# Kernel optimization log

Measured on AMD Instinct MI355X. Metric: run time of the kernel, lower is better.

Reference implementation:

```python
import jax, jax.numpy as jnp
import numpy as np

T, IN, M, C, OUT = 8192, 1024, 64, 16, 1024  # time, input, trace, context, output


def _ln(x, eps=1e-5):
    mu = jnp.mean(x, axis=-1, keepdims=True)
    var = jnp.var(x, axis=-1, keepdims=True)
    return (x - mu) * jax.lax.rsqrt(var + eps)


def _mish(x):
    return x * jnp.tanh(jax.nn.softplus(x))


def setup_inputs() -> dict:
    key = jax.random.key(0)
    ks = jax.random.split(key, 8)

    def w(k, o, i):
        return (jax.random.normal(k, (o, i), jnp.float32) / np.sqrt(i).astype(np.float32))

    return {
        "x": jax.random.normal(ks[0], (T, IN), jnp.float32),
        "state0": jnp.zeros((1, M, C), jnp.float32),  # real part of complex zero init
        "start": jax.random.uniform(ks[1], (T,)) < 0.002,  # sparse episode resets
        "next_done": jnp.zeros((T,), bool),  # unused by the sequential-equivalent math
        "a": jnp.linspace(1e-6, 0.5, M, dtype=jnp.float32),  # ffa.init decay
        "bf": (2.0 * jnp.pi / jnp.linspace(1.0, 1024.0, C)).astype(jnp.float32),  # ffa.init freqs
        "pre_w": w(ks[2], M, IN), "pre_b": jnp.zeros((M,), jnp.float32),
        "skip_w": w(ks[3], OUT, IN), "skip_b": jnp.zeros((OUT,), jnp.float32),
        "mix_w1": w(ks[4], M * C, 2 * M * C), "mix_b1": jnp.zeros((M * C,), jnp.float32),
        "mix_w2": w(ks[5], M * C, M * C), "mix_b2": jnp.zeros((M * C,), jnp.float32),
        "mix_w3": w(ks[6], OUT, M * C), "mix_b3": jnp.zeros((OUT,), jnp.float32),
    }


def _forward(x, state0, start, a, bf, pre_w, pre_b, skip_w, skip_b,
             mix_w1, mix_b1, mix_w2, mix_b2, mix_w3, mix_b3):
    Tn = x.shape[0]
    # pre = softplus(Linear(LayerNorm(x)))  -> [T, M]
    pre = jax.nn.softplus(_ln(x) @ pre_w.T + pre_b)
    # one-step FFA decay gamma[m,c] = exp(-|a_m| + i*b_c)
    la = jnp.broadcast_to(-jnp.abs(a)[:, None], (a.shape[0], bf.shape[0]))
    lb = jnp.broadcast_to(bf[None, :], la.shape)
    gamma = jnp.exp(jax.lax.complex(la, lb))  # [M, C] complex64
    # reset monoid: s_t = A_t * s_{t-1} + b_t,  A_t = 0 where episode starts
    A = jnp.where(start[:, None, None], jnp.zeros((), gamma.dtype), gamma[None])  # [T,M,C]
    b_el = jnp.broadcast_to(pre[:, :, None].astype(gamma.dtype), A.shape)  # [T,M,C]
    s_init = state0.astype(gamma.dtype)  # [1, M, C]
    b_el = b_el.at[0].add(A[0] * s_init[0])  # fold carried state into first element

    def combine(lhs, rhs):
        Al, bl = lhs
        Ar, br = rhs
        return Ar * Al, Ar * bl + br

    _, s = jax.lax.associative_scan(combine, (A, b_el))  # s: [T, M, C] states at every t

    s_flat = s.reshape(Tn, M * C)
    # global (all-element) complex mean / real std normalization, as in the source
    scaled = (s_flat - jnp.mean(s_flat)) / (1e-6 + jnp.std(s_flat))
    z = jnp.concatenate([scaled.real, scaled.imag], axis=-1)  # [T, 2*M*C]
    z = _mish(z @ mix_w1.T + mix_b1)
    z = _mish(z @ mix_w2.T + mix_b2)
    z = z @ mix_w3.T + mix_b3  # [T, OUT]
    out = _ln(z + (x @ skip_w.T + skip_b))
    return out, s[-1:]


def reference(x, state0, start, next_done, a, bf, pre_w, pre_b, skip_w, skip_b,
              mix_w1, mix_b1, mix_w2, mix_b2, mix_w3, mix_b3):
    return _forward(x, state0, start, a, bf, pre_w, pre_b, skip_w, skip_b,
                    mix_w1, mix_b1, mix_w2, mix_b2, mix_w3, mix_b3)
```

## Files before the change

### kernel.cpp

```cpp
#include <hip/hip_runtime.h>
#include <hip/hip_bf16.h>

#define T_    8192
#define INDIM 1024
#define MTR   64
#define CCTX  16
#define MC    1024
#define NOUT  1024
#define CHUNK 64
#define NCH   128

using bf16x8 = __attribute__((ext_vector_type(8))) short;
using f32x4  = __attribute__((ext_vector_type(4))) float;

__device__ __forceinline__ unsigned short f2bf(float f) {
  unsigned int u = __builtin_bit_cast(unsigned int, f);
  u += 0x7fffu + ((u >> 16) & 1u);
  return (unsigned short)(u >> 16);
}

__device__ __forceinline__ float mish_f(float v) {
  float u = __expf(v);
  float w = u * (u + 2.f);
  return (v > 20.f) ? v : v * __fdividef(w, w + 2.f);
}

typedef __attribute__((address_space(1))) void gas_void;
typedef __attribute__((address_space(3))) void las_void;

__device__ __forceinline__ void gload_lds16(const void* g, void* l) {
  __builtin_amdgcn_global_load_lds((gas_void*)g, (las_void*)l, 16, 0, 0);
}

__global__ __launch_bounds__(256) void cast4_k(const float* __restrict__ w1, const float* __restrict__ w2,
                                               const float* __restrict__ w3, const float* __restrict__ sw,
                                               unsigned short* __restrict__ o1, unsigned short* __restrict__ o2,
                                               unsigned short* __restrict__ o3, unsigned short* __restrict__ o4) {
  long i = ((long)blockIdx.x * 256 + threadIdx.x) * 4;
  const float* src; unsigned short* dst; long off;
  if (i < 2097152)      { src = w1; dst = o1; off = i; }
  else if (i < 3145728) { src = w2; dst = o2; off = i - 2097152; }
  else if (i < 4194304) { src = w3; dst = o3; off = i - 3145728; }
  else if (i < 5242880) { src = sw; dst = o4; off = i - 4194304; }
  else return;
  float4 v = *(const float4*)(src + off);
  ushort4 o = { f2bf(v.x), f2bf(v.y), f2bf(v.z), f2bf(v.w) };
  *(ushort4*)(dst + off) = o;
}

__device__ __forceinline__ float2 block_sum2(float s, float ss, float* sbuf) {
#pragma unroll
  for (int off = 32; off > 0; off >>= 1) {
    s  += __shfl_down(s, off);
    ss += __shfl_down(ss, off);
  }
  if ((threadIdx.x & 63) == 0) {
    sbuf[(threadIdx.x >> 6) * 2]     = s;
    sbuf[(threadIdx.x >> 6) * 2 + 1] = ss;
  }
  __syncthreads();
  return make_float2(sbuf[0] + sbuf[2] + sbuf[4] + sbuf[6],
                     sbuf[1] + sbuf[3] + sbuf[5] + sbuf[7]);
}

__global__ __launch_bounds__(256) void wsum_k(const float* __restrict__ w1,
                                              float* __restrict__ wre, float* __restrict__ wim) {
  __shared__ float sbuf[8];
  const long row = blockIdx.x;
  const float4* r4 = (const float4*)(w1 + row * 2048);
  float4 a = r4[threadIdx.x];
  float4 b = r4[256 + threadIdx.x];
  float2 t = block_sum2(a.x + a.y + a.z + a.w, b.x + b.y + b.z + b.w, sbuf);
  if (threadIdx.x == 0) { wre[row] = t.x; wim[row] = t.y; }
}

__global__ __launch_bounds__(256) void ln_cast_k(const float* __restrict__ x,
                                                 float2* __restrict__ rowstat,
                                                 unsigned short* __restrict__ xb) {
  __shared__ float sbuf[8];
  const long row = blockIdx.x;
  float4 v = ((const float4*)(x + (row << 10)))[threadIdx.x];
  ushort4 c = { f2bf(v.x), f2bf(v.y), f2bf(v.z), f2bf(v.w) };
  ((ushort4*)(xb + (row << 10)))[threadIdx.x] = c;
  float2 t = block_sum2(v.x + v.y + v.z + v.w,
                        v.x * v.x + v.y * v.y + v.z * v.z + v.w * v.w, sbuf);
  float mean = t.x * (1.f / 1024.f);
  float var  = t.y * (1.f / 1024.f) - mean * mean;
  float rstd = rsqrtf(var + 1e-5f);
  if (threadIdx.x == 0) rowstat[row] = make_float2(mean, rstd);
}

__global__ __launch_bounds__(256) void ln_out1_k(const float* __restrict__ p, float* __restrict__ out) {
  __shared__ float sbuf[8];
  const long row = blockIdx.x;
  float4 v = ((const float4*)(p + (row << 10)))[threadIdx.x];
  float2 t = block_sum2(v.x + v.y + v.z + v.w,
                        v.x * v.x + v.y * v.y + v.z * v.z + v.w * v.w, sbuf);
  float mean = t.x * (1.f / 1024.f);
  float var  = t.y * (1.f / 1024.f) - mean * mean;
  float rstd = rsqrtf(var + 1e-5f);
  float4 o = { (v.x - mean) * rstd, (v.y - mean) * rstd,
               (v.z - mean) * rstd, (v.w - mean) * rstd };
  ((float4*)(out + (row << 10)))[threadIdx.x] = o;
}

__global__ __launch_bounds__(256) void pre_part_k(const float* __restrict__ x,
                                                  const float2* __restrict__ rowstat,
                                                  const float* __restrict__ pw,
                                                  float* __restrict__ part) {
  const int lane = threadIdx.x & 63;
  const int wvu  = __builtin_amdgcn_readfirstlane(threadIdx.x >> 6);
  const int kc   = blockIdx.y;
  const int r0   = (blockIdx.x * 4 + wvu) * 32;

  const float* wrow = pw + (long)lane * 1024 + kc * 128;
  float wreg[128];
#pragma unroll
  for (int j = 0; j < 32; ++j)
    *(float4*)&wreg[j * 4] = ((const float4*)wrow)[j];
  float swsum = 0.f;
#pragma unroll
  for (int j = 0; j < 128; ++j) swsum += wreg[j];

  float* po = part + ((long)kc * T_ + r0) * 64 + lane;
  const float* xbase = x + (long)r0 * 1024 + kc * 128;

  for (int i = 0; i < 32; i += 2) {
    const float4* xr0 = (const float4*)(xbase + (long)i * 1024);
    const float4* xr1 = (const float4*)(xbase + (long)(i + 1) * 1024);
    float a0 = 0.f, a1 = 0.f, a2 = 0.f, a3 = 0.f;
    float b0 = 0.f, b1 = 0.f, b2 = 0.f, b3 = 0.f;
#pragma unroll
    for (int j = 0; j < 32; j += 4) {
      float4 xa0 = xr0[j],     xa1 = xr0[j + 1], xa2 = xr0[j + 2], xa3 = xr0[j + 3];
      float4 xb0 = xr1[j],     xb1 = xr1[j + 1], xb2 = xr1[j + 2], xb3 = xr1[j + 3];
      a0 += wreg[4*j+0]*xa0.x  + wreg[4*j+1]*xa0.y  + wreg[4*j+2]*xa0.z  + wreg[4*j+3]*xa0.w;
      a1 += wreg[4*j+4]*xa1.x  + wreg[4*j+5]*xa1.y  + wreg[4*j+6]*xa1.z  + wreg[4*j+7]*xa1.w;
      a2 += wreg[4*j+8]*xa2.x  + wreg[4*j+9]*xa2.y  + wreg[4*j+10]*xa2.z + wreg[4*j+11]*xa2.w;
      a3 += wreg[4*j+12]*xa3.x + wreg[4*j+13]*xa3.y + wreg[4*j+14]*xa3.z + wreg[4*j+15]*xa3.w;
      b0 += wreg[4*j+0]*xb0.x  + wreg[4*j+1]*xb0.y  + wreg[4*j+2]*xb0.z  + wreg[4*j+3]*xb0.w;
      b1 += wreg[4*j+4]*xb1.x  + wreg[4*j+5]*xb1.y  + wreg[4*j+6]*xb1.z  + wreg[4*j+7]*xb1.w;
      b2 += wreg[4*j+8]*xb2.x  + wreg[4*j+9]*xb2.y  + wreg[4*j+10]*xb2.z + wreg[4*j+11]*xb2.w;
      b3 += wreg[4*j+12]*xb3.x + wreg[4*j+13]*xb3.y + wreg[4*j+14]*xb3.z + wreg[4*j+15]*xb3.w;
    }
    float2 s0 = rowstat[r0 + i];
    float2 s1 = rowstat[r0 + i + 1];
    po[(long)i * 64]       = s0.y * ((a0 + a1) + (a2 + a3)) - s0.x * s0.y * swsum;
    po[(long)(i + 1) * 64] = s1.y * ((b0 + b1) + (b2 + b3)) - s1.x * s1.y * swsum;
  }
}

__global__ __launch_bounds__(256) void pre_fin_k(const float* __restrict__ part,
                                                 const float* __restrict__ pb,
                                                 float* __restrict__ pre) {
  long i = (long)blockIdx.x * 256 + threadIdx.x;
  int m = (int)(i & 63);
  float s = 0.f;
#pragma unroll
  for (int kc = 0; kc < 8; ++kc)
    s += part[(long)kc * T_ * 64 + i];
  float v = s + pb[m];
  float sp = fmaxf(v, 0.f) + log1pf(expf(-fabsf(v)));
  pre[i] = sp;
}

__global__ __launch_bounds__(256) void scan_p1(const float* __restrict__ pre, const int* __restrict__ start,
                                               const float* __restrict__ a, const float* __restrict__ bfr,
                                               double2* __restrict__ chA, double2* __restrict__ chB) {
  int ch = blockIdx.y * 256 + threadIdx.x;
  int m = ch >> 4, c = ch & 15;
  double dec = exp(-fabs((double)a[m]));
  double th = (double)bfr[c];
  double gre = dec * cos(th), gim = dec * sin(th);
  int j = blockIdx.x;
  int t0 = j * CHUNK;
  double pr = 1.0, pi = 0.0, sr = 0.0, si = 0.0;
  for (int t = t0; t < t0 + CHUNK; ++t) {
    double b = (double)pre[(long)t * 64 + m];
    if (start[t]) {
      pr = 0.0; pi = 0.0; sr = b; si = 0.0;
    } else {
      double nsr = gre * sr - gim * si + b;
      si = gre * si + gim * sr; sr = nsr;
      double npr = gre * pr - gim * pi;
      pi = gre * pi + gim * pr; pr = npr;
    }
  }
  chA[j * MC + ch] = make_double2(pr, pi);
  chB[j * MC + ch] = make_double2(sr, si);
}

__global__ __launch_bounds__(64) void scan_p2(const double2* __restrict__ chA, const double2* __restrict__ chB,
                                              const float* __restrict__ state0,
                                              double2* __restrict__ carry, double* __restrict__ red,
                                              float* __restrict__ out_tail, int fmt) {
  if (blockIdx.x == 0 && threadIdx.x < 4) red[threadIdx.x] = 0.0;
  int ch = blockIdx.x * 64 + threadIdx.x;
  double cr = (double)state0[ch], ci = 0.0;
  for (int j = 0; j < NCH; ++j) {
    carry[j * MC + ch] = make_double2(cr, ci);
    double2 A = chA[j * MC + ch];
    double2 B = chB[j * MC + ch];
    double ncr = A.x * cr - A.y * ci + B.x;
    ci = A.x * ci + A.y * cr + B.y;
    cr = ncr;
  }
  if (fmt == 1024) {
    out_tail[ch] = (float)cr;
  } else {
    out_tail[2 * ch]     = (float)cr;
    out_tail[2 * ch + 1] = (float)ci;
  }
}

__global__ __launch_bounds__(256) void scan_p3(const float* __restrict__ pre, const int* __restrict__ start,
                                               const float* __restrict__ a, const float* __restrict__ bfr,
                                               const double2* __restrict__ carry,
                                               double* __restrict__ red,
                                               unsigned short* __restrict__ z) {
  __shared__ double sbuf[12];
  int ch = blockIdx.y * 256 + threadIdx.x;
  int m = ch >> 4, c = ch & 15;
  double dec = exp(-fabs((double)a[m]));
  double th = (double)bfr[c];
  double gre = dec * cos(th), gim = dec * sin(th);
  int j = blockIdx.x;
  int t0 = j * CHUNK;
  double2 cin = carry[j * MC + ch];
  double sr = cin.x, si = cin.y;
  double aR = 0.0, aI = 0.0, aS = 0.0;
  for (int t = t0; t < t0 + CHUNK; ++t) {
    double b = (double)pre[(long)t * 64 + m];
    if (start[t]) { sr = b; si = 0.0; }
    else {
      double nsr = gre * sr - gim * si + b;
      si = gre * si + gim * sr; sr = nsr;
    }
    z[(long)t * 2048 + ch]        = f2bf((float)sr);
    z[(long)t * 2048 + 1024 + ch] = f2bf((float)si);
    aR += sr; aI += si; aS += sr * sr + si * si;
  }
#pragma unroll
  for (int off = 32; off > 0; off >>= 1) {
    aR += __shfl_down(aR, off); aI += __shfl_down(aI, off); aS += __shfl_down(aS, off);
  }
  if ((threadIdx.x & 63) == 0) {
    int w = threadIdx.x >> 6;
    sbuf[w * 3] = aR; sbuf[w * 3 + 1] = aI; sbuf[w * 3 + 2] = aS;
  }
  __syncthreads();
  if (threadIdx.x == 0) {
    atomicAdd(&red[0], sbuf[0] + sbuf[3] + sbuf[6] + sbuf[9]);
    atomicAdd(&red[1], sbuf[1] + sbuf[4] + sbuf[7] + sbuf[10]);
    atomicAdd(&red[2], sbuf[2] + sbuf[5] + sbuf[8] + sbuf[11]);
  }
}

__global__ void finalize_red(const double* __restrict__ red, float* __restrict__ redf) {
  const double n = (double)T_ * (double)MC;
  double mre = red[0] / n, mim = red[1] / n;
  double var = red[2] / n - mre * mre - mim * mim;
  double sd = sqrt(var > 0.0 ? var : 0.0);
  redf[0] = (float)mre;
  redf[1] = (float)mim;
  redf[2] = (float)(1.0 / (1e-6 + sd));
}

#define TSZ (128 * 32)
template<int EP>
__device__ __forceinline__ void gemm128_core(const unsigned short* __restrict__ A,
                                             const unsigned short* __restrict__ B,
                                             const float* __restrict__ bias,
                                             const float* __restrict__ add,
                                             const float* __restrict__ redf,
                                             const float* __restrict__ wre,
                                             const float* __restrict__ wim,
                                             void* __restrict__ Cout,
                                             int bx, int by, int N_, int K_,
                                             unsigned short* lA, unsigned short* lB) {
  const int tid = threadIdx.x;
  const int lane = tid & 63;
  const int wv = tid >> 6;
  const int wr = wv >> 1, wc = wv & 1;
  const long brow = (long)bx * 128;
  const long bcol = (long)by * 128;

  f32x4 acc[4][4];
#pragma unroll
  for (int i = 0; i < 4; i++)
#pragma unroll
    for (int j = 0; j < 4; j++)
      acc[i][j] = f32x4{0.f, 0.f, 0.f, 0.f};

  const int c0 = tid, c1 = tid + 256;
  const long ar0 = brow + (c0 >> 2), ar1 = brow + (c1 >> 2);
  const long br0 = bcol + (c0 >> 2), br1 = bcol + (c1 >> 2);
  const int ko0 = (((c0 & 3) ^ ((c0 >> 3) & 3)) * 8);
  const int ko1 = (((c1 & 3) ^ ((c1 >> 3) & 3)) * 8);
  const int r15 = lane & 15;
  const int swzq = (((lane >> 4) ^ ((r15 >> 1) & 3)) * 8);

  const int nt = K_ >> 5;

#define STAGE(ti, bu)                                                      \
  do {                                                                     \
    gload_lds16(A + ar0 * K_ + (ti) * 32 + ko0, lA + (bu) * TSZ + c0 * 8); \
    gload_lds16(A + ar1 * K_ + (ti) * 32 + ko1, lA + (bu) * TSZ + c1 * 8); \
    gload_lds16(B + br0 * K_ + (ti) * 32 + ko0, lB + (bu) * TSZ + c0 * 8); \
    gload_lds16(B + br1 * K_ + (ti) * 32 + ko1, lB + (bu) * TSZ + c1 * 8); \
  } while (0)

  STAGE(0, 0);
  STAGE(1, 1);

  int use = 0, stg = 2;
  for (int i = 0; i < nt; ++i) {
    if (i + 2 < nt) {
      STAGE(i + 2, stg);
      asm volatile("s_waitcnt vmcnt(8)" ::: "memory");
    } else if (i + 1 < nt) {
      asm volatile("s_waitcnt vmcnt(4)" ::: "memory");
    } else {
      asm volatile("s_waitcnt vmcnt(0)" ::: "memory");
    }
    __builtin_amdgcn_sched_barrier(0);
    __builtin_amdgcn_s_barrier();
    __builtin_amdgcn_sched_barrier(0);

    const unsigned short* bA = lA + use * TSZ;
    const unsigned short* bB = lB + use * TSZ;
    bf16x8 af[4], bv[4];
#pragma unroll
    for (int mi = 0; mi < 4; mi++)
      af[mi] = *(const bf16x8*)&bA[(wr * 64 + mi * 16 + r15) * 32 + swzq];
#pragma unroll
    for (int nj = 0; nj < 4; nj++)
      bv[nj] = *(const bf16x8*)&bB[(wc * 64 + nj * 16 + r15) * 32 + swzq];
#pragma unroll
    for (int mi = 0; mi < 4; mi++)
#pragma unroll
      for (int nj = 0; nj < 4; nj++)
        acc[mi][nj] = __builtin_amdgcn_mfma_f32_16x16x32_bf16(af[mi], bv[nj], acc[mi][nj], 0, 0, 0);

    __builtin_amdgcn_sched_barrier(0);
    __builtin_amdgcn_s_barrier();
    use = (use == 2) ? 0 : use + 1;
    stg = (stg == 2) ? 0 : stg + 1;
  }
#undef STAGE

  float cre = 0.f, cim = 0.f, inv = 1.f;
  if (EP == 4) { cre = redf[0]; cim = redf[1]; inv = redf[2]; }

  const int rq = (lane >> 4) * 4;
#pragma unroll
  for (int nj = 0; nj < 4; nj++) {
    const long col = bcol + wc * 64 + nj * 16 + r15;
    const float bs = bias[col];
    float wrc = 0.f, wic = 0.f;
    if (EP == 4) { wrc = wre[col]; wic = wim[col]; }
#pragma unroll
    for (int mi = 0; mi < 4; mi++) {
#pragma unroll
      for (int r = 0; r < 4; r++) {
        const long row = brow + wr * 64 + mi * 16 + rq + r;
        float va = acc[mi][nj][r];
        if (EP == 0) {
          ((float*)Cout)[row * N_ + col] = va + bs;
        } else if (EP == 3) {
          ((float*)Cout)[row * N_ + col] = va + bs + add[row * N_ + col];
        } else if (EP == 4) {
          float v = (va - cre * wrc - cim * wic) * inv + bs;
          ((unsigned short*)Cout)[row * N_ + col] = f2bf(mish_f(v));
        } else {
          ((unsigned short*)Cout)[row * N_ + col] = f2bf(mish_f(va + bs));
        }
      }
    }
  }
}

template<int EP>
__global__ __launch_bounds__(256) void gemm128_k(const unsigned short* __restrict__ A,
                                                 const unsigned short* __restrict__ B,
                                                 const float* __restrict__ bias,
                                                 const float* __restrict__ add,
                                                 void* __restrict__ Cout, int N_, int K_) {
  __shared__ __align__(16) unsigned short lA[3 * TSZ];
  __shared__ __align__(16) unsigned short lB[3 * TSZ];
  gemm128_core<EP>(A, B, bias, add, nullptr, nullptr, nullptr, Cout,
                   blockIdx.x, blockIdx.y, N_, K_, lA, lB);
}

__global__ __launch_bounds__(256) void gemm_dual128(const unsigned short* __restrict__ A1,
                                                    const unsigned short* __restrict__ B1,
                                                    const float* __restrict__ bias1,
                                                    unsigned short* __restrict__ C1, int K1,
                                                    const float* __restrict__ redf,
                                                    const float* __restrict__ wre,
                                                    const float* __restrict__ wim,
                                                    const unsigned short* __restrict__ A2,
                                                    const unsigned short* __restrict__ B2,
                                                    const float* __restrict__ bias2,
                                                    float* __restrict__ C2, int K2) {
  __shared__ __align__(16) unsigned short lA[3 * TSZ];
  __shared__ __align__(16) unsigned short lB[3 * TSZ];
  int b = blockIdx.x;
  if (b < 512) {
    gemm128_core<4>(A1, B1, bias1, nullptr, redf, wre, wim, C1, b & 63, b >> 6, 1024, K1, lA, lB);
  } else {
    b -= 512;
    gemm128_core<0>(A2, B2, bias2, nullptr, nullptr, nullptr, nullptr, C2, b & 63, b >> 6, 1024, K2, lA, lB);
  }
}

extern "C" void kernel_launch(void* const* d_in, const int* in_sizes, int n_in,
                              void* d_out, int out_size, void* d_ws, size_t ws_size,
                              hipStream_t stream) {
  (void)in_sizes; (void)n_in; (void)ws_size;
  const float* x      = (const float*)d_in[0];
  const float* state0 = (const float*)d_in[1];
  const int*   start  = (const int*)d_in[2];
  const float* a      = (const float*)d_in[4];
  const float* bfr    = (const float*)d_in[5];
  const float* pre_w  = (const float*)d_in[6];
  const float* pre_b  = (const float*)d_in[7];
  const float* skip_w = (const float*)d_in[8];
  const float* skip_b = (const float*)d_in[9];
  const float* w1     = (const float*)d_in[10];
  const float* b1     = (const float*)d_in[11];
  const float* w2     = (const float*)d_in[12];
  const float* b2     = (const float*)d_in[13];
  const float* w3     = (const float*)d_in[14];
  const float* b3     = (const float*)d_in[15];

  char* ws = (char*)d_ws;
  const size_t MB = 1u << 20;
  float*          skipf = (float*)(ws + 0);
  float*          part  = (float*)(ws + 32 * MB);
  float*          h3    = (float*)(ws + 32 * MB);
  unsigned short* z     = (unsigned short*)(ws + 64 * MB);
  unsigned short* xb    = (unsigned short*)(ws + 96 * MB);
  unsigned short* h2    = (unsigned short*)(ws + 96 * MB);
  unsigned short* h1    = (unsigned short*)(ws + 112 * MB);
  unsigned short* wb1   = (unsigned short*)(ws + 128 * MB);
  unsigned short* wb2   = (unsigned short*)(ws + 132 * MB);
  unsigned short* wb3   = (unsigned short*)(ws + 134 * MB);
  unsigned short* skwb  = (unsigned short*)(ws + 136 * MB);
  float*          pre   = (float*)(ws + 138 * MB);
  double2*        chA   = (double2*)(ws + 140 * MB);
  double2*        chB   = (double2*)(ws + 142 * MB);
  double2*        carry = (double2*)(ws + 144 * MB);
  double*         red   = (double*)(ws + 146 * MB);
  float*          redf  = (float*)(ws + 146 * MB + 64);
  float2*         rowst = (float2*)(ws + 147 * MB);
  float*          wre   = (float*)(ws + 147 * MB + 65536);
  float*          wim   = (float*)(ws + 147 * MB + 65536 + 4096);

  cast4_k<<<5120, 256, 0, stream>>>(w1, w2, w3, skip_w, wb1, wb2, wb3, skwb);
  wsum_k<<<1024, 256, 0, stream>>>(w1, wre, wim);

  ln_cast_k<<<8192, 256, 0, stream>>>(x, rowst, xb);
  pre_part_k<<<dim3(64, 8), 256, 0, stream>>>(x, rowst, pre_w, part);
  pre_fin_k<<<2048, 256, 0, stream>>>(part, pre_b, pre);

  int tail_elems = out_size - T_ * NOUT;
  float* out_tail = (float*)d_out + (long)T_ * NOUT;
  scan_p1<<<dim3(NCH, 4), 256, 0, stream>>>(pre, start, a, bfr, chA, chB);
  scan_p2<<<16, 64, 0, stream>>>(chA, chB, state0, carry, red, out_tail, tail_elems);
  scan_p3<<<dim3(NCH, 4), 256, 0, stream>>>(pre, start, a, bfr, carry, red, z);
  finalize_red<<<1, 1, 0, stream>>>(red, redf);

  gemm_dual128<<<1024, 256, 0, stream>>>(z, wb1, b1, h1, 2048, redf, wre, wim,
                                         xb, skwb, skip_b, skipf, 1024);
  gemm128_k<2><<<dim3(64, 8), 256, 0, stream>>>(h1, wb2, b2, nullptr, h2, 1024, 1024);
  gemm128_k<3><<<dim3(64, 8), 256, 0, stream>>>(h2, wb3, b3, skipf, h3, 1024, 1024);

  ln_out1_k<<<8192, 256, 0, stream>>>(h3, (float*)d_out);
}
```

Baseline: 296.7 us.

## Store skip and pre-LN outputs in bf16 and use 4-buffer LDS ring with one barrier

The skip GEMM output and the final pre-LayerNorm activation are now written and read as bf16 instead of fp32, which halves the global traffic for these two 32 MB intermediates. The GEMM LDS pipeline goes from 3 to 4 buffers indexed by i&3, so the trailing barrier per k-step can be dropped. The cost is reduced precision ahead of the final LayerNorm and more LDS per block, which may lower occupancy.

Result: faster. 277.9 us (-6.3%).

```diff
diff --git a/kernel.cpp b/kernel.cpp
--- a/kernel.cpp
+++ b/kernel.cpp
@@ -17,6 +17,9 @@
   unsigned int u = __builtin_bit_cast(unsigned int, f);
   u += 0x7fffu + ((u >> 16) & 1u);
   return (unsigned short)(u >> 16);
+}
+__device__ __forceinline__ float bf2f(unsigned short u) {
+  return __builtin_bit_cast(float, (unsigned int)u << 16);
 }
 
 __device__ __forceinline__ float mish_f(float v) {
@@ -90,10 +93,11 @@
   if (threadIdx.x == 0) rowstat[row] = make_float2(mean, rstd);
 }
 
-__global__ __launch_bounds__(256) void ln_out1_k(const float* __restrict__ p, float* __restrict__ out) {
+__global__ __launch_bounds__(256) void ln_out1b_k(const unsigned short* __restrict__ p, float* __restrict__ out) {
   __shared__ float sbuf[8];
   const long row = blockIdx.x;
-  float4 v = ((const float4*)(p + (row << 10)))[threadIdx.x];
+  ushort4 u4 = ((const ushort4*)(p + (row << 10)))[threadIdx.x];
+  float4 v = { bf2f(u4.x), bf2f(u4.y), bf2f(u4.z), bf2f(u4.w) };
   float2 t = block_sum2(v.x + v.y + v.z + v.w,
                         v.x * v.x + v.y * v.y + v.z * v.z + v.w * v.w, sbuf);
   float mean = t.x * (1.f / 1024.f);
@@ -271,7 +275,7 @@
 __device__ __forceinline__ void gemm128_core(const unsigned short* __restrict__ A,
                                              const unsigned short* __restrict__ B,
                                              const float* __restrict__ bias,
-                                             const float* __restrict__ add,
+                                             const unsigned short* __restrict__ addb,
                                              const float* __restrict__ redf,
                                              const float* __restrict__ wre,
                                              const float* __restrict__ wim,
@@ -313,10 +317,9 @@
   STAGE(0, 0);
   STAGE(1, 1);
 
-  int use = 0, stg = 2;
   for (int i = 0; i < nt; ++i) {
     if (i + 2 < nt) {
-      STAGE(i + 2, stg);
+      STAGE(i + 2, (i + 2) & 3);
       asm volatile("s_waitcnt vmcnt(8)" ::: "memory");
     } else if (i + 1 < nt) {
       asm volatile("s_waitcnt vmcnt(4)" ::: "memory");
@@ -327,8 +330,8 @@
     __builtin_amdgcn_s_barrier();
     __builtin_amdgcn_sched_barrier(0);
 
-    const unsigned short* bA = lA + use * TSZ;
-    const unsigned short* bB = lB + use * TSZ;
+    const unsigned short* bA = lA + (i & 3) * TSZ;
+    const unsigned short* bB = lB + (i & 3) * TSZ;
     bf16x8 af[4], bv[4];
 #pragma unroll
     for (int mi = 0; mi < 4; mi++)
@@ -341,11 +344,6 @@
 #pragma unroll
       for (int nj = 0; nj < 4; nj++)
         acc[mi][nj] = __builtin_amdgcn_mfma_f32_16x16x32_bf16(af[mi], bv[nj], acc[mi][nj], 0, 0, 0);
-
-    __builtin_amdgcn_sched_barrier(0);
-    __builtin_amdgcn_s_barrier();
-    use = (use == 2) ? 0 : use + 1;
-    stg = (stg == 2) ? 0 : stg + 1;
   }
 #undef STAGE
 
@@ -365,10 +363,11 @@
       for (int r = 0; r < 4; r++) {
         const long row = brow + wr * 64 + mi * 16 + rq + r;
         float va = acc[mi][nj][r];
-        if (EP == 0) {
-          ((float*)Cout)[row * N_ + col] = va + bs;
+        if (EP == 1) {
+          ((unsigned short*)Cout)[row * N_ + col] = f2bf(va + bs);
         } else if (EP == 3) {
-          ((float*)Cout)[row * N_ + col] = va + bs + add[row * N_ + col];
+          float v = va + bs + bf2f(addb[row * N_ + col]);
+          ((unsigned short*)Cout)[row * N_ + col] = f2bf(v);
         } else if (EP == 4) {
           float v = (va - cre * wrc - cim * wic) * inv + bs;
           ((unsigned short*)Cout)[row * N_ + col] = f2bf(mish_f(v));
@@ -384,11 +383,11 @@
 __global__ __launch_bounds__(256) void gemm128_k(const unsigned short* __restrict__ A,
                                                  const unsigned short* __restrict__ B,
                                                  const float* __restrict__ bias,
-                                                 const float* __restrict__ add,
+                                                 const unsigned short* __restrict__ addb,
                                                  void* __restrict__ Cout, int N_, int K_) {
-  __shared__ __align__(16) unsigned short lA[3 * TSZ];
-  __shared__ __align__(16) unsigned short lB[3 * TSZ];
-  gemm128_core<EP>(A, B, bias, add, nullptr, nullptr, nullptr, Cout,
+  __shared__ __align__(16) unsigned short lA[4 * TSZ];
+  __shared__ __align__(16) unsigned short lB[4 * TSZ];
+  gemm128_core<EP>(A, B, bias, addb, nullptr, nullptr, nullptr, Cout,
                    blockIdx.x, blockIdx.y, N_, K_, lA, lB);
 }
 
@@ -402,15 +401,15 @@
                                                     const unsigned short* __restrict__ A2,
                                                     const unsigned short* __restrict__ B2,
                                                     const float* __restrict__ bias2,
-                                                    float* __restrict__ C2, int K2) {
-  __shared__ __align__(16) unsigned short lA[3 * TSZ];
-  __shared__ __align__(16) unsigned short lB[3 * TSZ];
+                                                    unsigned short* __restrict__ C2, int K2) {
+  __shared__ __align__(16) unsigned short lA[4 * TSZ];
+  __shared__ __align__(16) unsigned short lB[4 * TSZ];
   int b = blockIdx.x;
   if (b < 512) {
     gemm128_core<4>(A1, B1, bias1, nullptr, redf, wre, wim, C1, b & 63, b >> 6, 1024, K1, lA, lB);
   } else {
     b -= 512;
-    gemm128_core<0>(A2, B2, bias2, nullptr, nullptr, nullptr, nullptr, C2, b & 63, b >> 6, 1024, K2, lA, lB);
+    gemm128_core<1>(A2, B2, bias2, nullptr, nullptr, nullptr, nullptr, C2, b & 63, b >> 6, 1024, K2, lA, lB);
   }
 }
 
@@ -436,9 +435,9 @@
 
   char* ws = (char*)d_ws;
   const size_t MB = 1u << 20;
-  float*          skipf = (float*)(ws + 0);
+  unsigned short* skipb = (unsigned short*)(ws + 0);
   float*          part  = (float*)(ws + 32 * MB);
-  float*          h3    = (float*)(ws + 32 * MB);
+  unsigned short* h3b   = (unsigned short*)(ws + 48 * MB);
   unsigned short* z     = (unsigned short*)(ws + 64 * MB);
   unsigned short* xb    = (unsigned short*)(ws + 96 * MB);
   unsigned short* h2    = (unsigned short*)(ws + 96 * MB);
@@ -472,9 +471,9 @@
   finalize_red<<<1, 1, 0, stream>>>(red, redf);
 
   gemm_dual128<<<1024, 256, 0, stream>>>(z, wb1, b1, h1, 2048, redf, wre, wim,
-                                         xb, skwb, skip_b, skipf, 1024);
+                                         xb, skwb, skip_b, skipb, 1024);
   gemm128_k<2><<<dim3(64, 8), 256, 0, stream>>>(h1, wb2, b2, nullptr, h2, 1024, 1024);
-  gemm128_k<3><<<dim3(64, 8), 256, 0, stream>>>(h2, wb3, b3, skipf, h3, 1024, 1024);
-
-  ln_out1_k<<<8192, 256, 0, stream>>>(h3, (float*)d_out);
-}
+  gemm128_k<3><<<dim3(64, 8), 256, 0, stream>>>(h2, wb3, b3, skipb, h3b, 1024, 1024);
+
+  ln_out1b_k<<<8192, 256, 0, stream>>>(h3b, (float*)d_out);
+}
```
